# Optimization experiments

Hardware: AMD Instinct MI355X
Metric: run time of the kernel (lower is better)

Reference implementation:

```python
import jax, jax.numpy as jnp
import numpy as np

N, E = 50000, 800000
F_NODE, F_EDGE, H, LAT, MAXN = 128, 16, 128, 64, 200


def setup_inputs() -> dict:
    key = jax.random.key(0)
    ks = jax.random.split(key, 40)
    s = 0.05
    p = {
        'x': jax.random.normal(ks[0], (N, F_NODE), jnp.float32),
        'edge_index': jax.random.randint(ks[1], (2, E), 0, N, jnp.int64),
        'edge_attr': jax.random.normal(ks[2], (E, F_EDGE), jnp.float32),
        'eps': jax.random.normal(ks[3], (1, LAT), jnp.float32),
        'num_nodes': N,
        # GATConv layer 1 (heads=1)
        'W1': jax.random.normal(ks[4], (F_NODE, H), jnp.float32) * s,
        'att_src1': jax.random.normal(ks[5], (H,), jnp.float32) * s,
        'att_dst1': jax.random.normal(ks[6], (H,), jnp.float32) * s,
        'We1': jax.random.normal(ks[7], (F_EDGE, H), jnp.float32) * s,
        'att_e1': jax.random.normal(ks[8], (H,), jnp.float32) * s,
        'b1': jnp.zeros((H,), jnp.float32),
        # GATConv layer 2
        'W2': jax.random.normal(ks[9], (H, H), jnp.float32) * s,
        'att_src2': jax.random.normal(ks[10], (H,), jnp.float32) * s,
        'att_dst2': jax.random.normal(ks[11], (H,), jnp.float32) * s,
        'We2': jax.random.normal(ks[12], (F_EDGE, H), jnp.float32) * s,
        'att_e2': jax.random.normal(ks[13], (H,), jnp.float32) * s,
        'b2': jnp.zeros((H,), jnp.float32),
        # heads
        'mu_W': jax.random.normal(ks[14], (H, LAT), jnp.float32) * s,
        'mu_b': jnp.zeros((LAT,), jnp.float32),
        'lv_W': jax.random.normal(ks[15], (H, LAT), jnp.float32) * s,
        'lv_b': jnp.zeros((LAT,), jnp.float32),
        'dec_W': jax.random.normal(ks[16], (LAT, H), jnp.float32) * s,
        'dec_b': jnp.zeros((H,), jnp.float32),
        'adj_W1': jax.random.normal(ks[17], (H, H), jnp.float32) * s,
        'adj_b1': jnp.zeros((H,), jnp.float32),
        'adj_W2': jax.random.normal(ks[18], (H, MAXN), jnp.float32) * s,
        'adj_b2': jnp.zeros((MAXN,), jnp.float32),
        'nd_W1': jax.random.normal(ks[19], (H, H), jnp.float32) * s,
        'nd_b1': jnp.zeros((H,), jnp.float32),
        'nd_W2': jax.random.normal(ks[20], (H, F_NODE), jnp.float32) * s,
        'nd_b2': jnp.zeros((F_NODE,), jnp.float32),
    }
    return p


def _gat(h, src, dst, ea, W, a_s, a_d, We, a_e, b, n):
    # PyG GATConv, heads=1: linear transform, per-edge attention, segment softmax over dst
    g = h @ W                                     # [n, H]
    alpha = jax.nn.leaky_relu((g @ a_s)[src] + (g @ a_d)[dst] + (ea @ We) @ a_e,
                              negative_slope=0.2)  # [E']
    m = jax.ops.segment_max(alpha, dst, num_segments=n)
    ex = jnp.exp(alpha - m[dst])
    den = jax.ops.segment_sum(ex, dst, num_segments=n)
    w = ex / den[dst]
    return jax.ops.segment_sum(w[:, None] * g[src], dst, num_segments=n) + b


def _forward(x, edge_index, edge_attr, eps, num_nodes,
             W1, att_src1, att_dst1, We1, att_e1, b1,
             W2, att_src2, att_dst2, We2, att_e2, b2,
             mu_W, mu_b, lv_W, lv_b, dec_W, dec_b,
             adj_W1, adj_b1, adj_W2, adj_b2, nd_W1, nd_b1, nd_W2, nd_b2):
    n = x.shape[0]
    src, dst = edge_index[0], edge_index[1]
    # add self loops; self-loop edge_attr = per-node mean of incoming edge_attr (PyG fill_value='mean')
    deg = jax.ops.segment_sum(jnp.ones((src.shape[0],), x.dtype), dst, num_segments=n)
    mean_ea = jax.ops.segment_sum(edge_attr, dst, num_segments=n) / jnp.maximum(deg, 1.0)[:, None]
    loop = jnp.arange(n)
    src_f = jnp.concatenate([src, loop])
    dst_f = jnp.concatenate([dst, loop])
    ea_f = jnp.concatenate([edge_attr, mean_ea])
    h = jax.nn.relu(_gat(x, src_f, dst_f, ea_f, W1, att_src1, att_dst1, We1, att_e1, b1, n))
    h = jax.nn.relu(_gat(h, src_f, dst_f, ea_f, W2, att_src2, att_dst2, We2, att_e2, b2, n))
    hg = h.mean(axis=0, keepdims=True)            # global_mean_pool, single graph -> [1, H]
    mu = hg @ mu_W + mu_b
    logvar = hg @ lv_W + lv_b
    z = mu + eps * jnp.exp(0.5 * logvar)
    hd = jax.nn.relu(z @ dec_W + dec_b)           # [1, H]
    hn = jnp.broadcast_to(hd[:, None, :], (1, num_nodes, hd.shape[-1]))
    adj = jax.nn.relu(hn @ adj_W1 + adj_b1) @ adj_W2 + adj_b2   # [1, n, MAXN]
    adj = adj[:, :, :num_nodes]
    nodes = jax.nn.relu(hn @ nd_W1 + nd_b1) @ nd_W2 + nd_b2     # [1, n, F_NODE]
    return adj, nodes, mu, logvar


def reference(x, edge_index, edge_attr, eps, num_nodes,
              W1, att_src1, att_dst1, We1, att_e1, b1,
              W2, att_src2, att_dst2, We2, att_e2, b2,
              mu_W, mu_b, lv_W, lv_b, dec_W, dec_b,
              adj_W1, adj_b1, adj_W2, adj_b2, nd_W1, nd_b1, nd_W2, nd_b2):
    return _forward(x, edge_index, edge_attr, eps, num_nodes,
                    W1, att_src1, att_dst1, We1, att_e1, b1,
                    W2, att_src2, att_dst2, We2, att_e2, b2,
                    mu_W, mu_b, lv_W, lv_b, dec_W, dec_b,
                    adj_W1, adj_b1, adj_W2, adj_b2, nd_W1, nd_b1, nd_W2, nd_b2)
```

## Files before the change

kernel.cpp:

```cpp
#include <hip/hip_runtime.h>
#include <math.h>

#define NN   50000
#define EE   800000
#define EF   850000
#define HH   128
#define FE   16
#define LATD 64
#define MAXNN 200

#define ADJ_TOT   10000000
#define NODES_TOT 6400000
#define OUT_TOT   16400000
#define MU_OFF    16400000
#define LV_OFF    16400064

#define GEMMBLOCKS 782
#define DEGBLOCKS  782
#define NBSCAN     49
#define FLAGBIT    0x80000000u

typedef __attribute__((ext_vector_type(8))) short bf16x8;
typedef __attribute__((ext_vector_type(4))) float f32x4;
typedef __attribute__((ext_vector_type(2))) float f32x2;

__device__ __forceinline__ unsigned short f2bf(float f){
  unsigned int u = __float_as_uint(f);
  unsigned int r = (u + 0x7FFFu + ((u>>16)&1u)) >> 16;
  return (unsigned short)r;
}
__device__ __forceinline__ float bf2f(unsigned short h){
  return __uint_as_float(((unsigned int)h)<<16);
}

__global__ __launch_bounds__(256) void kprep(int* ideg, float* hgsum, unsigned* scanpub,
                       const float* We1, const float* ae1, const float* We2, const float* ae2,
                       float* wa1, float* wa2,
                       const float* W1, const float* W2,
                       unsigned short* Wp1, unsigned short* Wp2){
  int i = blockIdx.x*256 + threadIdx.x;
  if(i < NN) ideg[i]=0;
  if(i < HH) hgsum[i]=0.f;
  if(i < 64) scanpub[i]=0u;
  if(i < FE){
    float s1=0.f, s2=0.f;
    for(int j=0;j<HH;j++){ s1 += We1[i*HH+j]*ae1[j]; s2 += We2[i*HH+j]*ae2[j]; }
    wa1[i]=s1; wa2[i]=s2;
  }
  if(i < HH*HH){
    int n = i >> 7, k = i & 127;
    Wp1[i] = f2bf(W1[k*HH + n]);
    Wp2[i] = f2bf(W2[k*HH + n]);
  }
}

__device__ __forceinline__ void gemm_body(int bid, int tid, const void* __restrict__ hin, int h_is_fp32,
    const unsigned short* __restrict__ Wp,
    const float* __restrict__ atts, const float* __restrict__ attd,
    unsigned char* __restrict__ A8, float* __restrict__ asrc, float* __restrict__ adst){
  int lane = tid & 63;
  int wid  = tid >> 6;
  int l = lane & 15, q = lane >> 4;
  int r0 = bid*64 + wid*16;
  if(r0 >= NN) return;
  const unsigned short* hb = (const unsigned short*)hin;
  const float*          hf = (const float*)hin;
  int row = r0 + l;

  bf16x8 afr[4];
  if(h_is_fp32){
    float4 u[8];
    #pragma unroll
    for(int kb=0;kb<4;kb++){
      const float* p = hf + (size_t)row*HH + kb*32 + q*8;
      u[kb*2]   = *(const float4*)(p);
      u[kb*2+1] = *(const float4*)(p+4);
    }
    #pragma unroll
    for(int kb=0;kb<4;kb++){
      afr[kb][0]=(short)f2bf(u[kb*2].x);   afr[kb][1]=(short)f2bf(u[kb*2].y);
      afr[kb][2]=(short)f2bf(u[kb*2].z);   afr[kb][3]=(short)f2bf(u[kb*2].w);
      afr[kb][4]=(short)f2bf(u[kb*2+1].x); afr[kb][5]=(short)f2bf(u[kb*2+1].y);
      afr[kb][6]=(short)f2bf(u[kb*2+1].z); afr[kb][7]=(short)f2bf(u[kb*2+1].w);
    }
  } else {
    #pragma unroll
    for(int kb=0;kb<4;kb++)
      afr[kb] = *(const bf16x8*)(hb + (size_t)row*HH + kb*32 + q*8);
  }

  f32x4 acc[8];
  #pragma unroll
  for(int t=0;t<8;t++) acc[t]=(f32x4){0.f,0.f,0.f,0.f};

  #pragma unroll
  for(int kb=0;kb<4;kb++){
    #pragma unroll
    for(int t=0;t<8;t++){
      bf16x8 b = *(const bf16x8*)(Wp + (size_t)(t*16+l)*HH + kb*32 + q*8);
      acc[t] = __builtin_amdgcn_mfma_f32_16x16x32_bf16(afr[kb], b, acc[t], 0,0,0);
    }
  }

  float av[8], dv[8];
  #pragma unroll
  for(int t=0;t<8;t++){ av[t]=atts[t*16+l]; dv[t]=attd[t*16+l]; }
  #pragma unroll
  for(int reg=0;reg<4;reg++){
    float ps=0.f, pd=0.f;
    #pragma unroll
    for(int t=0;t<8;t++){ ps+=acc[t][reg]*av[t]; pd+=acc[t][reg]*dv[t]; }
    #pragma unroll
    for(int m=8;m>=1;m>>=1){ ps+=__shfl_xor(ps,m,16); pd+=__shfl_xor(pd,m,16); }
    if(l==0){ int R=r0+q*4+reg; asrc[R]=ps; adst[R]=pd; }
  }
  #pragma unroll
  for(int t=0;t<8;t++)
    #pragma unroll
    for(int reg=0;reg<4;reg++){
      int pk = __builtin_amdgcn_cvt_pk_fp8_f32(acc[t][reg], 0.f, 0, false);
      A8[(size_t)(r0+q*4+reg)*HH + t*16 + l] = (unsigned char)(pk & 0xFF);
    }
}

__global__ __launch_bounds__(256) void kgemm3(const void* __restrict__ hin, int h_is_fp32,
    const unsigned short* __restrict__ Wp,
    const float* __restrict__ atts, const float* __restrict__ attd,
    unsigned char* __restrict__ A8, float* __restrict__ asrc, float* __restrict__ adst){
  gemm_body(blockIdx.x, threadIdx.x, hin, h_is_fp32, Wp, atts, attd, A8, asrc, adst);
}

__device__ __forceinline__ unsigned etpack(const float4* a4,
                         const float* __restrict__ wa1, const float* __restrict__ wa2){
  float4 v0=a4[0], v1=a4[1], v2=a4[2], v3=a4[3];
  float va[16]={v0.x,v0.y,v0.z,v0.w, v1.x,v1.y,v1.z,v1.w,
                v2.x,v2.y,v2.z,v2.w, v3.x,v3.y,v3.z,v3.w};
  float d1=0.f,d2=0.f;
  #pragma unroll
  for(int f=0;f<FE;f++){ d1+=va[f]*wa1[f]; d2+=va[f]*wa2[f]; }
  return (unsigned)f2bf(d1) | ((unsigned)f2bf(d2)<<16);
}

__global__ __launch_bounds__(256) void kdeggemm(
    const int* __restrict__ ei, int* ideg, unsigned short* __restrict__ erank,
    const float* __restrict__ ea, const float* __restrict__ wa1, const float* __restrict__ wa2,
    unsigned* __restrict__ ety,
    const void* __restrict__ hin, int h_is_fp32,
    const unsigned short* __restrict__ Wp,
    const float* __restrict__ atts, const float* __restrict__ attd,
    unsigned char* __restrict__ A8, float* __restrict__ asrc, float* __restrict__ adst){
  if(blockIdx.x < GEMMBLOCKS){
    gemm_body(blockIdx.x, threadIdx.x, hin, h_is_fp32, Wp, atts, attd, A8, asrc, adst);
  } else {
    int e0 = ((blockIdx.x - GEMMBLOCKS)*256 + threadIdx.x)*4;
    if(e0 + 3 < EE){
      int4 d4 = *(const int4*)(ei + EE + e0);
      unsigned short r0 = (unsigned short)atomicAdd(&ideg[d4.x], 1);
      unsigned short r1 = (unsigned short)atomicAdd(&ideg[d4.y], 1);
      unsigned short r2 = (unsigned short)atomicAdd(&ideg[d4.z], 1);
      unsigned short r3 = (unsigned short)atomicAdd(&ideg[d4.w], 1);
      const float4* a4 = (const float4*)(ea + (size_t)e0*FE);
      uint4 y;
      y.x = etpack(a4,    wa1, wa2);
      y.y = etpack(a4+4,  wa1, wa2);
      y.z = etpack(a4+8,  wa1, wa2);
      y.w = etpack(a4+12, wa1, wa2);
      *(uint4*)(ety + e0) = y;
      ushort4 rr; rr.x=r0; rr.y=r1; rr.z=r2; rr.w=r3;
      *(ushort4*)(erank + e0) = rr;
    }
  }
}

__global__ void kscanf(const int* __restrict__ ideg, int* __restrict__ rowstart,
                       unsigned* __restrict__ scanpub){
  __shared__ int sd[1024];
  __shared__ int bo[64];
  int t=threadIdx.x, b=blockIdx.x;
  int i = b*1024 + t;
  int v = (i<NN)? (ideg[i]+1) : 0;
  sd[t]=v; __syncthreads();
  for(int off=1; off<1024; off<<=1){
    int x=(t>=off)? sd[t-off]:0; __syncthreads();
    sd[t]+=x; __syncthreads();
  }
  if(t==1023) atomicExch(&scanpub[b], (unsigned)sd[1023] | FLAGBIT);
  if(t<64){
    int j = (t<NBSCAN)? t : NBSCAN-1;
    unsigned u;
    do { u = atomicAdd(&scanpub[j], 0u); } while(!(u & FLAGBIT));
    int agg = (t<NBSCAN)? (int)(u & ~FLAGBIT) : 0;
    int inc = agg;
    #pragma unroll
    for(int off=1; off<64; off<<=1){
      int x = __shfl_up(inc, off);
      if(t>=off) inc += x;
    }
    bo[t] = inc - agg;
  }
  __syncthreads();
  if(i<NN) rowstart[i] = sd[t]-v + bo[b];
  if(b==0 && t==0) rowstart[NN] = bo[NBSCAN];
}

__global__ __launch_bounds__(256) void kscatter(const int* __restrict__ ei,
                         const unsigned* __restrict__ ety,
                         const int* __restrict__ rowstart,
                         const unsigned short* __restrict__ erank,
                         uint2* __restrict__ csr){
  int e0 = (blockIdx.x*256 + threadIdx.x)*4;
  if(e0 >= EE) return;
  int4 s4 = *(const int4*)(ei + e0);
  int4 d4 = *(const int4*)(ei + EE + e0);
  ushort4 r4 = *(const ushort4*)(erank + e0);
  uint4 y4 = *(const uint4*)(ety + e0);
  uint2 en;
  en.x=(unsigned)s4.x; en.y=y4.x; csr[rowstart[d4.x]+(int)r4.x]=en;
  en.x=(unsigned)s4.y; en.y=y4.y; csr[rowstart[d4.y]+(int)r4.y]=en;
  en.x=(unsigned)s4.z; en.y=y4.z; csr[rowstart[d4.z]+(int)r4.z]=en;
  en.x=(unsigned)s4.w; en.y=y4.w; csr[rowstart[d4.w]+(int)r4.w]=en;
}

__global__ __launch_bounds__(256) void kgat(const unsigned char* __restrict__ A8,
    const float* __restrict__ asrc, const float* __restrict__ adst,
    const int* __restrict__ rowstart, uint2* __restrict__ csr,
    int mode, const float* __restrict__ bias,
    float* __restrict__ alphabuf, int* __restrict__ srcbuf,
    unsigned short* __restrict__ Bout){
  int lane = threadIdx.x & 63;
  int wid  = threadIdx.x >> 6;
  int half = lane >> 5;
  int hl   = lane & 31;
  int i = blockIdx.x*8 + wid*2 + half;
  if(i >= NN) return;
  int base = rowstart[i];
  int len  = rowstart[i+1]-base;
  float adi = adst[i];
  int lq = hl & 15;
  int qq = hl >> 4;
  float av[8];
  #pragma unroll
  for(int j=0;j<8;j++) av[j]=0.f;

  if(__builtin_expect(len <= 32, 1)){
    int P2 = (len+1)>>1;
    int nread = mode ? len : len-1;
    int s = i; float etlo = 0.f, ethi = 0.f;
    if(hl < nread){
      uint2 en = csr[base+hl];
      s = (int)en.x;
      etlo = bf2f((unsigned short)(en.y & 0xFFFFu));
      ethi = bf2f((unsigned short)(en.y >> 16));
    }
    float et = mode ? ethi : etlo;
    int skv0[6];
    #pragma unroll
    for(int j=0;j<6;j++) skv0[j] = (j<P2) ? __shfl(s, 2*j+qq, 32) : i;
    unsigned ux[6], uy[6];
    #pragma unroll
    for(int j=0;j<6;j++){
      uint2 u = *(const uint2*)(A8 + (size_t)skv0[j]*HH + lq*8);
      ux[j]=u.x; uy[j]=u.y;
    }
    if(!mode){
      float e1 = (hl < len-1) ? etlo : 0.f;
      float e2 = (hl < len-1) ? ethi : 0.f;
      #pragma unroll
      for(int mk=16;mk>=1;mk>>=1){ e1 += __shfl_xor(e1,mk); e2 += __shfl_xor(e2,mk); }
      float dg = fmaxf((float)(len-1), 1.f);
      float m1 = e1/dg, m2 = e2/dg;
      if(hl == len-1){
        et = m1;
        uint2 se; se.x=(unsigned)i;
        se.y=(unsigned)f2bf(m1) | ((unsigned)f2bf(m2)<<16);
        csr[base+len-1] = se;
      }
    }
    float a = -1e30f;
    if(hl < len){
      a = asrc[s] + adi + et;
      a = fmaxf(a, 0.2f*a);
    }
    float m = a;
    #pragma unroll
    for(int mk=16;mk>=1;mk>>=1) m = fmaxf(m, __shfl_xor(m,mk));
    float ex = (hl<len) ? __expf(a-m) : 0.f;
    float sm = ex;
    #pragma unroll
    for(int mk=16;mk>=1;mk>>=1) sm += __shfl_xor(sm,mk);
    ex *= __builtin_amdgcn_rcpf(sm);

    float w0[6];
    #pragma unroll
    for(int j=0;j<6;j++) w0[j] = (j<P2) ? __shfl(ex, 2*j+qq, 32) : 0.f;
    #pragma unroll
    for(int j=0;j<6;j++){
      f32x2 v;
      v=__builtin_amdgcn_cvt_pk_f32_fp8((int)ux[j],false); av[0]+=w0[j]*v[0]; av[1]+=w0[j]*v[1];
      v=__builtin_amdgcn_cvt_pk_f32_fp8((int)ux[j],true ); av[2]+=w0[j]*v[0]; av[3]+=w0[j]*v[1];
      v=__builtin_amdgcn_cvt_pk_f32_fp8((int)uy[j],false); av[4]+=w0[j]*v[0]; av[5]+=w0[j]*v[1];
      v=__builtin_amdgcn_cvt_pk_f32_fp8((int)uy[j],true ); av[6]+=w0[j]*v[0]; av[7]+=w0[j]*v[1];
    }
    for(int t0=6; t0<P2; t0+=6){
      int skv[6]; float w[6];
      #pragma unroll
      for(int j=0;j<6;j++){
        if(t0+j < P2){
          int idx = 2*(t0+j) + qq;
          skv[j] = __shfl(s, idx, 32);
          w[j]   = __shfl(ex, idx, 32);
        } else { skv[j] = i; w[j] = 0.f; }
      }
      unsigned vx[6], vy[6];
      #pragma unroll
      for(int j=0;j<6;j++){
        uint2 u = *(const uint2*)(A8 + (size_t)skv[j]*HH + lq*8);
        vx[j]=u.x; vy[j]=u.y;
      }
      #pragma unroll
      for(int j=0;j<6;j++){
        f32x2 v;
        v=__builtin_amdgcn_cvt_pk_f32_fp8((int)vx[j],false); av[0]+=w[j]*v[0]; av[1]+=w[j]*v[1];
        v=__builtin_amdgcn_cvt_pk_f32_fp8((int)vx[j],true ); av[2]+=w[j]*v[0]; av[3]+=w[j]*v[1];
        v=__builtin_amdgcn_cvt_pk_f32_fp8((int)vy[j],false); av[4]+=w[j]*v[0]; av[5]+=w[j]*v[1];
        v=__builtin_amdgcn_cvt_pk_f32_fp8((int)vy[j],true ); av[6]+=w[j]*v[0]; av[7]+=w[j]*v[1];
      }
    }
  } else {
    int deg = len-1;
    int lim = mode ? len : deg;
    float lm = -1e30f, e1 = 0.f, e2 = 0.f;
    for(int k=hl;k<lim;k+=32){
      uint2 en = csr[base+k];
      int sr = (int)en.x;
      float lo = bf2f((unsigned short)(en.y & 0xFFFFu));
      float hi = bf2f((unsigned short)(en.y >> 16));
      float etv = mode ? hi : lo;
      if(!mode){ e1 += lo; e2 += hi; }
      float a = asrc[sr] + adi + etv;
      a = fmaxf(a, 0.2f*a);
      alphabuf[base+k]=a; srcbuf[base+k]=sr;
      lm = fmaxf(lm,a);
    }
    #pragma unroll
    for(int mk=16;mk>=1;mk>>=1){
      e1 += __shfl_xor(e1,mk);
      e2 += __shfl_xor(e2,mk);
      lm  = fmaxf(lm, __shfl_xor(lm,mk));
    }
    float aself = 0.f;
    if(!mode){
      float m1 = e1/(float)deg, m2 = e2/(float)deg;
      aself = asrc[i] + adi + m1;
      aself = fmaxf(aself, 0.2f*aself);
      lm = fmaxf(lm, aself);
      if(hl==0){
        uint2 se; se.x=(unsigned)i;
        se.y=(unsigned)f2bf(m1) | ((unsigned)f2bf(m2)<<16);
        csr[base+deg] = se;
      }
    }
    float ls=0.f;
    for(int k=hl;k<len;k+=32){
      float a;
      if(mode) a = alphabuf[base+k];
      else     a = (k<deg)? alphabuf[base+k] : aself;
      float e_ = __expf(a-lm);
      alphabuf[base+k]=e_;
      ls += e_;
    }
    #pragma unroll
    for(int mk=16;mk>=1;mk>>=1) ls += __shfl_xor(ls,mk);
    float inv = 1.f/ls;
    int lim2 = mode ? len : deg;
    int P2 = (len+1)>>1;
    for(int t=0;t<P2;t++){
      int k = 2*t + qq;
      int sk = i; float wk = 0.f;
      if(k<len){
        sk = (k<lim2)? srcbuf[base+k] : i;
        wk = alphabuf[base+k]*inv;
      }
      uint2 u = *(const uint2*)(A8 + (size_t)sk*HH + lq*8);
      f32x2 v;
      v=__builtin_amdgcn_cvt_pk_f32_fp8((int)u.x,false); av[0]+=wk*v[0]; av[1]+=wk*v[1];
      v=__builtin_amdgcn_cvt_pk_f32_fp8((int)u.x,true ); av[2]+=wk*v[0]; av[3]+=wk*v[1];
      v=__builtin_amdgcn_cvt_pk_f32_fp8((int)u.y,false); av[4]+=wk*v[0]; av[5]+=wk*v[1];
      v=__builtin_amdgcn_cvt_pk_f32_fp8((int)u.y,true ); av[6]+=wk*v[0]; av[7]+=wk*v[1];
    }
  }

  #pragma unroll
  for(int j=0;j<8;j++) av[j] += __shfl_xor(av[j],16);
  if(qq==0){
    const float4* bp = (const float4*)(bias + lq*8);
    float4 b0=bp[0], b1=bp[1];
    float o0=fmaxf(av[0]+b0.x,0.f), o1=fmaxf(av[1]+b0.y,0.f);
    float o2=fmaxf(av[2]+b0.z,0.f), o3=fmaxf(av[3]+b0.w,0.f);
    float o4=fmaxf(av[4]+b1.x,0.f), o5=fmaxf(av[5]+b1.y,0.f);
    float o6=fmaxf(av[6]+b1.z,0.f), o7=fmaxf(av[7]+b1.w,0.f);
    uint4 ov;
    ov.x=(unsigned)f2bf(o0)|((unsigned)f2bf(o1)<<16);
    ov.y=(unsigned)f2bf(o2)|((unsigned)f2bf(o3)<<16);
    ov.z=(unsigned)f2bf(o4)|((unsigned)f2bf(o5)<<16);
    ov.w=(unsigned)f2bf(o6)|((unsigned)f2bf(o7)<<16);
    *(uint4*)(Bout + (size_t)i*HH + lq*8) = ov;
  }
}

__global__ __launch_bounds__(256) void khg(const unsigned short* __restrict__ B, float* hgsum){
  int f = threadIdx.x & 127;
  int half = threadIdx.x >> 7;
  float s=0.f;
  for(int i = blockIdx.x*2+half; i < NN; i += gridDim.x*2)
    s += bf2f(B[(size_t)i*HH + f]);
  __shared__ float sd[256];
  sd[threadIdx.x]=s; __syncthreads();
  if(half==0) atomicAdd(&hgsum[f], sd[threadIdx.x]+sd[threadIdx.x+128]);
}

__global__ __launch_bounds__(256) void kdec(const float* __restrict__ hgsum, const float* __restrict__ eps,
   const float* muW,const float* mub,const float* lvW,const float* lvb,
   const float* decW,const float* decb,
   const float* aW1,const float* ab1,const float* aW2,const float* ab2,
   const float* nW1,const float* nb1,const float* nW2,const float* nb2,
   float* out, float* rowadj, float* rownodes){
  __shared__ float hg[HH], z[LATD], hd[HH], t1[HH], t2[HH];
  int t=threadIdx.x;
  if(t<HH) hg[t]=hgsum[t]*(1.0f/NN);
  __syncthreads();
  if(t<LATD){
    float mu=mub[t], lv=lvb[t];
    #pragma unroll 8
    for(int k=0;k<HH;k++){ mu += hg[k]*muW[k*LATD+t]; lv += hg[k]*lvW[k*LATD+t]; }
    out[MU_OFF+t]=mu; out[LV_OFF+t]=lv;
    z[t]=mu + eps[t]*expf(0.5f*lv);
  }
  __syncthreads();
  if(t<HH){
    float a=decb[t];
    #pragma unroll 8
    for(int k=0;k<LATD;k++) a += z[k]*decW[k*HH+t];
    hd[t]=fmaxf(a,0.f);
  }
  __syncthreads();
  if(t<HH){
    float a=ab1[t];
    #pragma unroll 8
    for(int k=0;k<HH;k++) a += hd[k]*aW1[k*HH+t];
    t1[t]=fmaxf(a,0.f);
  } else {
    int j=t-HH;
    float a=nb1[j];
    #pragma unroll 8
    for(int k=0;k<HH;k++) a += hd[k]*nW1[k*HH+j];
    t2[j]=fmaxf(a,0.f);
  }
  __syncthreads();
  for(int j=t;j<MAXNN;j+=256){
    float a=ab2[j];
    #pragma unroll 8
    for(int k=0;k<HH;k++) a += t1[k]*aW2[k*MAXNN+j];
    rowadj[j]=a;
  }
  if(t<HH){
    float a=nb2[t];
    #pragma unroll 8
    for(int k=0;k<HH;k++) a += t2[k]*nW2[k*HH+t];
    rownodes[t]=a;
  }
}

__global__ __launch_bounds__(256) void kbcast(const float* __restrict__ rowadj,
                                              const float* __restrict__ rownodes,
                                              float* __restrict__ out){
  int lane = threadIdx.x & 63;
  int wv = (blockIdx.x*256 + threadIdx.x) >> 6;
  int nw = (gridDim.x*256) >> 6;
  float4 aseg = {0.f,0.f,0.f,0.f}, nseg = {0.f,0.f,0.f,0.f};
  if(lane<50) aseg = ((const float4*)rowadj)[lane];
  if(lane<32) nseg = ((const float4*)rownodes)[lane];
  for(int r=wv; r<NN; r+=nw)
    if(lane<50) *(float4*)(out + (size_t)r*MAXNN + lane*4) = aseg;
  for(int r=wv; r<NN; r+=nw)
    if(lane<32) *(float4*)(out + ADJ_TOT + (size_t)r*HH + lane*4) = nseg;
}

extern "C" void kernel_launch(void* const* d_in, const int* in_sizes, int n_in,
                              void* d_out, int out_size, void* d_ws, size_t ws_size,
                              hipStream_t stream){
  const float* x   = (const float*)d_in[0];
  const int*   ei  = (const int*)d_in[1];
  const float* ea  = (const float*)d_in[2];
  const float* eps = (const float*)d_in[3];
  const float* W1  =(const float*)d_in[5];
  const float* as1 =(const float*)d_in[6];
  const float* ad1 =(const float*)d_in[7];
  const float* We1 =(const float*)d_in[8];
  const float* ae1 =(const float*)d_in[9];
  const float* b1  =(const float*)d_in[10];
  const float* W2  =(const float*)d_in[11];
  const float* as2 =(const float*)d_in[12];
  const float* ad2 =(const float*)d_in[13];
  const float* We2 =(const float*)d_in[14];
  const float* ae2 =(const float*)d_in[15];
  const float* b2  =(const float*)d_in[16];
  const float* muW =(const float*)d_in[17];
  const float* mub =(const float*)d_in[18];
  const float* lvW =(const float*)d_in[19];
  const float* lvb =(const float*)d_in[20];
  const float* decW=(const float*)d_in[21];
  const float* decb=(const float*)d_in[22];
  const float* aW1 =(const float*)d_in[23];
  const float* ab1 =(const float*)d_in[24];
  const float* aW2 =(const float*)d_in[25];
  const float* ab2 =(const float*)d_in[26];
  const float* nW1 =(const float*)d_in[27];
  const float* nb1 =(const float*)d_in[28];
  const float* nW2 =(const float*)d_in[29];
  const float* nb2 =(const float*)d_in[30];
  float* out=(float*)d_out;

  char* w=(char*)d_ws;
  unsigned char*  A8  = (unsigned char*)w;  w += (size_t)NN*HH;
  unsigned short* Bbf = (unsigned short*)w; w += (size_t)NN*HH*2;
  unsigned short* Wp1 = (unsigned short*)w; w += (size_t)HH*HH*2;
  unsigned short* Wp2 = (unsigned short*)w; w += (size_t)HH*HH*2;
  uint2*  csr      = (uint2*)w;  w += (size_t)EF*8;
  float*  alphabuf = (float*)w;  w += (size_t)EF*4;
  int*    srcbuf   = (int*)w;    w += (size_t)EF*4;
  unsigned* ety    = (unsigned*)w; w += (size_t)EE*4;
  unsigned short* erank = (unsigned short*)w; w += (size_t)EE*2;
  int*    rowstart = (int*)w;    w += (size_t)(NN+1)*4;
  int*    ideg     = (int*)w;    w += (size_t)NN*4;
  float*  hgsum    = (float*)w;  w += 128*4;
  float*  asrc     = (float*)w;  w += (size_t)NN*4;
  float*  adst     = (float*)w;  w += (size_t)NN*4;
  float*  wa1      = (float*)w;  w += 16*4;
  float*  wa2      = (float*)w;  w += 16*4;
  float*  rowadj   = (float*)w;  w += 256*4;
  float*  rownodes = (float*)w;  w += 128*4;
  unsigned* scanpub= (unsigned*)w; w += 64*4;

  int gatblocks  = (NN+7)/8;

  hipLaunchKernelGGL(kprep, dim3((NN+255)/256), dim3(256), 0, stream,
                     ideg, hgsum, scanpub, We1, ae1, We2, ae2, wa1, wa2, W1, W2, Wp1, Wp2);
  hipLaunchKernelGGL(kdeggemm, dim3(GEMMBLOCKS+DEGBLOCKS), dim3(256), 0, stream,
                     ei, ideg, erank, ea, wa1, wa2, ety,
                     (const void*)x, 1, Wp1, as1, ad1, A8, asrc, adst);
  hipLaunchKernelGGL(kscanf, dim3(NBSCAN), dim3(1024), 0, stream, ideg, rowstart, scanpub);
  hipLaunchKernelGGL(kscatter, dim3((EE/4+255)/256), dim3(256), 0, stream,
                     ei, ety, rowstart, erank, csr);
  hipLaunchKernelGGL(kgat,  dim3(gatblocks), dim3(256), 0, stream,
                     A8, asrc, adst, rowstart, csr, 0, b1, alphabuf, srcbuf, Bbf);
  hipLaunchKernelGGL(kgemm3, dim3(GEMMBLOCKS), dim3(256), 0, stream,
                     (const void*)Bbf, 0, Wp2, as2, ad2, A8, asrc, adst);
  hipLaunchKernelGGL(kgat,  dim3(gatblocks), dim3(256), 0, stream,
                     A8, asrc, adst, rowstart, csr, 1, b2, alphabuf, srcbuf, Bbf);
  hipLaunchKernelGGL(khg,   dim3(512), dim3(256), 0, stream, Bbf, hgsum);
  hipLaunchKernelGGL(kdec,  dim3(1), dim3(256), 0, stream, hgsum, eps,
                     muW,mub,lvW,lvb,decW,decb,aW1,ab1,aW2,ab2,nW1,nb1,nW2,nb2,
                     out, rowadj, rownodes);
  hipLaunchKernelGGL(kbcast, dim3(2048), dim3(256), 0, stream, rowadj, rownodes, out);
}
```

Measured before the change: 399.0 us.

## Fuse whole pipeline into one cooperative persistent kernel with grid syncs

Replaces the chain of ten kernel launches with a single cooperative kernel that loops blocks over work units and separates stages with grid-wide syncs. The lookback scan becomes a two-level chunk scan, and the edge-attribute projection moves from the degree pass into the scatter pass, which drops the ety buffer. The intent is to cut launch gaps and tail effects between stages. In exchange, grid syncs add barrier cost, the persistent grid is capped by occupancy, and register pressure from the merged body may lower occupancy for the GAT and GEMM stages. A multi-kernel fallback is kept for devices without cooperative launch.

Result: slower. 862.0 us (+116.0%).

```diff
diff --git a/kernel.cpp b/kernel.cpp
--- a/kernel.cpp
+++ b/kernel.cpp
@@ -1,22 +1,26 @@
 #include <hip/hip_runtime.h>
+#include <hip/hip_cooperative_groups.h>
 #include <math.h>
+
+namespace cg = cooperative_groups;
 
 #define NN   50000
 #define EE   800000
-#define EF   850000
 #define HH   128
 #define FE   16
 #define LATD 64
 #define MAXNN 200
 
 #define ADJ_TOT   10000000
-#define NODES_TOT 6400000
 #define OUT_TOT   16400000
 #define MU_OFF    16400000
 #define LV_OFF    16400064
 
 #define GEMMBLOCKS 782
 #define DEGBLOCKS  782
+#define SCATUNITS  1563
+#define GATUNITS   6250
+#define NCHUNK     196
 #define NBSCAN     49
 #define FLAGBIT    0x80000000u
 
@@ -33,26 +37,6 @@
   return __uint_as_float(((unsigned int)h)<<16);
 }
 
-__global__ __launch_bounds__(256) void kprep(int* ideg, float* hgsum, unsigned* scanpub,
-                       const float* We1, const float* ae1, const float* We2, const float* ae2,
-                       float* wa1, float* wa2,
-                       const float* W1, const float* W2,
-                       unsigned short* Wp1, unsigned short* Wp2){
-  int i = blockIdx.x*256 + threadIdx.x;
-  if(i < NN) ideg[i]=0;
-  if(i < HH) hgsum[i]=0.f;
-  if(i < 64) scanpub[i]=0u;
-  if(i < FE){
-    float s1=0.f, s2=0.f;
-    for(int j=0;j<HH;j++){ s1 += We1[i*HH+j]*ae1[j]; s2 += We2[i*HH+j]*ae2[j]; }
-    wa1[i]=s1; wa2[i]=s2;
-  }
-  if(i < HH*HH){
-    int n = i >> 7, k = i & 127;
-    Wp1[i] = f2bf(W1[k*HH + n]);
-    Wp2[i] = f2bf(W2[k*HH + n]);
-  }
-}
 
 __device__ __forceinline__ void gemm_body(int bid, int tid, const void* __restrict__ hin, int h_is_fp32,
     const unsigned short* __restrict__ Wp,
@@ -123,11 +107,18 @@
     }
 }
 
-__global__ __launch_bounds__(256) void kgemm3(const void* __restrict__ hin, int h_is_fp32,
-    const unsigned short* __restrict__ Wp,
-    const float* __restrict__ atts, const float* __restrict__ attd,
-    unsigned char* __restrict__ A8, float* __restrict__ asrc, float* __restrict__ adst){
-  gemm_body(blockIdx.x, threadIdx.x, hin, h_is_fp32, Wp, atts, attd, A8, asrc, adst);
+__device__ __forceinline__ void deg_unit(int u, int tid,
+    const int* __restrict__ ei, int* ideg, unsigned short* __restrict__ erank){
+  int e0 = (u*256 + tid)*4;
+  if(e0 + 3 < EE){
+    int4 d4 = *(const int4*)(ei + EE + e0);
+    unsigned short r0 = (unsigned short)atomicAdd(&ideg[d4.x], 1);
+    unsigned short r1 = (unsigned short)atomicAdd(&ideg[d4.y], 1);
+    unsigned short r2 = (unsigned short)atomicAdd(&ideg[d4.z], 1);
+    unsigned short r3 = (unsigned short)atomicAdd(&ideg[d4.w], 1);
+    ushort4 rr; rr.x=r0; rr.y=r1; rr.z=r2; rr.w=r3;
+    *(ushort4*)(erank + e0) = rr;
+  }
 }
 
 __device__ __forceinline__ unsigned etpack(const float4* a4,
@@ -141,97 +132,36 @@
   return (unsigned)f2bf(d1) | ((unsigned)f2bf(d2)<<16);
 }
 
-__global__ __launch_bounds__(256) void kdeggemm(
-    const int* __restrict__ ei, int* ideg, unsigned short* __restrict__ erank,
-    const float* __restrict__ ea, const float* __restrict__ wa1, const float* __restrict__ wa2,
-    unsigned* __restrict__ ety,
-    const void* __restrict__ hin, int h_is_fp32,
-    const unsigned short* __restrict__ Wp,
-    const float* __restrict__ atts, const float* __restrict__ attd,
-    unsigned char* __restrict__ A8, float* __restrict__ asrc, float* __restrict__ adst){
-  if(blockIdx.x < GEMMBLOCKS){
-    gemm_body(blockIdx.x, threadIdx.x, hin, h_is_fp32, Wp, atts, attd, A8, asrc, adst);
-  } else {
-    int e0 = ((blockIdx.x - GEMMBLOCKS)*256 + threadIdx.x)*4;
-    if(e0 + 3 < EE){
-      int4 d4 = *(const int4*)(ei + EE + e0);
-      unsigned short r0 = (unsigned short)atomicAdd(&ideg[d4.x], 1);
-      unsigned short r1 = (unsigned short)atomicAdd(&ideg[d4.y], 1);
-      unsigned short r2 = (unsigned short)atomicAdd(&ideg[d4.z], 1);
-      unsigned short r3 = (unsigned short)atomicAdd(&ideg[d4.w], 1);
-      const float4* a4 = (const float4*)(ea + (size_t)e0*FE);
-      uint4 y;
-      y.x = etpack(a4,    wa1, wa2);
-      y.y = etpack(a4+4,  wa1, wa2);
-      y.z = etpack(a4+8,  wa1, wa2);
-      y.w = etpack(a4+12, wa1, wa2);
-      *(uint4*)(ety + e0) = y;
-      ushort4 rr; rr.x=r0; rr.y=r1; rr.z=r2; rr.w=r3;
-      *(ushort4*)(erank + e0) = rr;
-    }
-  }
-}
-
-__global__ void kscanf(const int* __restrict__ ideg, int* __restrict__ rowstart,
-                       unsigned* __restrict__ scanpub){
-  __shared__ int sd[1024];
-  __shared__ int bo[64];
-  int t=threadIdx.x, b=blockIdx.x;
-  int i = b*1024 + t;
-  int v = (i<NN)? (ideg[i]+1) : 0;
-  sd[t]=v; __syncthreads();
-  for(int off=1; off<1024; off<<=1){
-    int x=(t>=off)? sd[t-off]:0; __syncthreads();
-    sd[t]+=x; __syncthreads();
-  }
-  if(t==1023) atomicExch(&scanpub[b], (unsigned)sd[1023] | FLAGBIT);
-  if(t<64){
-    int j = (t<NBSCAN)? t : NBSCAN-1;
-    unsigned u;
-    do { u = atomicAdd(&scanpub[j], 0u); } while(!(u & FLAGBIT));
-    int agg = (t<NBSCAN)? (int)(u & ~FLAGBIT) : 0;
-    int inc = agg;
-    #pragma unroll
-    for(int off=1; off<64; off<<=1){
-      int x = __shfl_up(inc, off);
-      if(t>=off) inc += x;
-    }
-    bo[t] = inc - agg;
-  }
-  __syncthreads();
-  if(i<NN) rowstart[i] = sd[t]-v + bo[b];
-  if(b==0 && t==0) rowstart[NN] = bo[NBSCAN];
-}
-
-__global__ __launch_bounds__(256) void kscatter(const int* __restrict__ ei,
-                         const unsigned* __restrict__ ety,
-                         const int* __restrict__ rowstart,
-                         const unsigned short* __restrict__ erank,
-                         uint2* __restrict__ csr){
-  int e0 = (blockIdx.x*256 + threadIdx.x)*4;
+__device__ __forceinline__ void scat_unit(int u, int tid,
+    const int* __restrict__ ei, const float* __restrict__ ea,
+    const float* __restrict__ wa1, const float* __restrict__ wa2,
+    const int* __restrict__ rowstart, const unsigned short* __restrict__ erank,
+    uint2* __restrict__ csr){
+  int e0 = (u*256 + tid)*2;
   if(e0 >= EE) return;
-  int4 s4 = *(const int4*)(ei + e0);
-  int4 d4 = *(const int4*)(ei + EE + e0);
-  ushort4 r4 = *(const ushort4*)(erank + e0);
-  uint4 y4 = *(const uint4*)(ety + e0);
-  uint2 en;
-  en.x=(unsigned)s4.x; en.y=y4.x; csr[rowstart[d4.x]+(int)r4.x]=en;
-  en.x=(unsigned)s4.y; en.y=y4.y; csr[rowstart[d4.y]+(int)r4.y]=en;
-  en.x=(unsigned)s4.z; en.y=y4.z; csr[rowstart[d4.z]+(int)r4.z]=en;
-  en.x=(unsigned)s4.w; en.y=y4.w; csr[rowstart[d4.w]+(int)r4.w]=en;
-}
-
-__global__ __launch_bounds__(256) void kgat(const unsigned char* __restrict__ A8,
+  int sA=ei[e0],    sB=ei[e0+1];
+  int dA=ei[EE+e0], dB=ei[EE+e0+1];
+  int rA=(int)erank[e0], rB=(int)erank[e0+1];
+  int pA=rowstart[dA]+rA, pB=rowstart[dB]+rB;
+  const float4* a4 = (const float4*)(ea + (size_t)e0*FE);
+  unsigned yA = etpack(a4,   wa1, wa2);
+  unsigned yB = etpack(a4+4, wa1, wa2);
+  uint2 enA; enA.x=(unsigned)sA; enA.y=yA;
+  uint2 enB; enB.x=(unsigned)sB; enB.y=yB;
+  csr[pA]=enA; csr[pB]=enB;
+}
+
+__device__ void kgat_body(int unit, int tid, const unsigned char* __restrict__ A8,
     const float* __restrict__ asrc, const float* __restrict__ adst,
     const int* __restrict__ rowstart, uint2* __restrict__ csr,
     int mode, const float* __restrict__ bias,
     float* __restrict__ alphabuf, int* __restrict__ srcbuf,
     unsigned short* __restrict__ Bout){
-  int lane = threadIdx.x & 63;
-  int wid  = threadIdx.x >> 6;
+  int lane = tid & 63;
+  int wid  = tid >> 6;
   int half = lane >> 5;
   int hl   = lane & 31;
-  int i = blockIdx.x*8 + wid*2 + half;
+  int i = unit*8 + wid*2 + half;
   if(i >= NN) return;
   int base = rowstart[i];
   int len  = rowstart[i+1]-base;
@@ -408,25 +338,26 @@
   }
 }
 
-__global__ __launch_bounds__(256) void khg(const unsigned short* __restrict__ B, float* hgsum){
-  int f = threadIdx.x & 127;
-  int half = threadIdx.x >> 7;
+__device__ __forceinline__ void khg_unit(int u, int tid,
+    const unsigned short* __restrict__ B, float* hgsum, float* sfd){
+  int f = tid & 127;
+  int half = tid >> 7;
   float s=0.f;
-  for(int i = blockIdx.x*2+half; i < NN; i += gridDim.x*2)
+  for(int i = u*2+half; i < NN; i += 1024)
     s += bf2f(B[(size_t)i*HH + f]);
-  __shared__ float sd[256];
-  sd[threadIdx.x]=s; __syncthreads();
-  if(half==0) atomicAdd(&hgsum[f], sd[threadIdx.x]+sd[threadIdx.x+128]);
-}
-
-__global__ __launch_bounds__(256) void kdec(const float* __restrict__ hgsum, const float* __restrict__ eps,
+  sfd[tid]=s; __syncthreads();
+  if(half==0) atomicAdd(&hgsum[f], sfd[tid]+sfd[tid+128]);
+  __syncthreads();
+}
+
+__device__ void dec_body(int tid, const float* __restrict__ hgsum, const float* __restrict__ eps,
    const float* muW,const float* mub,const float* lvW,const float* lvb,
    const float* decW,const float* decb,
    const float* aW1,const float* ab1,const float* aW2,const float* ab2,
    const float* nW1,const float* nb1,const float* nW2,const float* nb2,
-   float* out, float* rowadj, float* rownodes){
-  __shared__ float hg[HH], z[LATD], hd[HH], t1[HH], t2[HH];
-  int t=threadIdx.x;
+   float* out, float* rowadj, float* rownodes,
+   float* hg, float* z, float* hd, float* t1, float* t2){
+  int t=tid;
   if(t<HH) hg[t]=hgsum[t]*(1.0f/NN);
   __syncthreads();
   if(t<LATD){
@@ -471,12 +402,9 @@
   }
 }
 
-__global__ __launch_bounds__(256) void kbcast(const float* __restrict__ rowadj,
-                                              const float* __restrict__ rownodes,
-                                              float* __restrict__ out){
-  int lane = threadIdx.x & 63;
-  int wv = (blockIdx.x*256 + threadIdx.x) >> 6;
-  int nw = (gridDim.x*256) >> 6;
+__device__ __forceinline__ void bcast_wave(int wv, int nw, int lane,
+    const float* __restrict__ rowadj, const float* __restrict__ rownodes,
+    float* __restrict__ out){
   float4 aseg = {0.f,0.f,0.f,0.f}, nseg = {0.f,0.f,0.f,0.f};
   if(lane<50) aseg = ((const float4*)rowadj)[lane];
   if(lane<32) nseg = ((const float4*)rownodes)[lane];
@@ -485,6 +413,210 @@
   for(int r=wv; r<NN; r+=nw)
     if(lane<32) *(float4*)(out + ADJ_TOT + (size_t)r*HH + lane*4) = nseg;
 }
+
+
+struct MP {
+  const float *x; const int *ei; const float *ea; const float *eps;
+  const float *W1,*as1,*ad1,*We1,*ae1,*b1;
+  const float *W2,*as2,*ad2,*We2,*ae2,*b2;
+  const float *muW,*mub,*lvW,*lvb,*decW,*decb;
+  const float *aW1,*ab1,*aW2,*ab2,*nW1,*nb1,*nW2,*nb2;
+  float *out;
+  unsigned char *A8; unsigned short *Bbf, *Wp1, *Wp2;
+  uint2 *csr; float *alphabuf; int *srcbuf; unsigned short *erank;
+  int *rowstart, *ideg; float *hgsum, *asrc, *adst, *wa1, *wa2, *rowadj, *rownodes;
+  int *chunksum, *chunkoff;
+};
+
+__global__ __launch_bounds__(256) void kmega(MP p){
+  cg::grid_group grid = cg::this_grid();
+  const int nb  = gridDim.x;
+  const int tid = threadIdx.x;
+  const int gid = blockIdx.x*256 + tid;
+  const int gsz = nb*256;
+  __shared__ int   sd[256];
+  __shared__ float sfd[256];
+  __shared__ float shg[HH], sz[LATD], shd[HH], st1[HH], st2[HH];
+
+  for(int i=gid; i<NN; i+=gsz) p.ideg[i]=0;
+  for(int i=gid; i<HH; i+=gsz) p.hgsum[i]=0.f;
+  for(int i=gid; i<FE; i+=gsz){
+    float s1=0.f, s2=0.f;
+    for(int j=0;j<HH;j++){ s1 += p.We1[i*HH+j]*p.ae1[j]; s2 += p.We2[i*HH+j]*p.ae2[j]; }
+    p.wa1[i]=s1; p.wa2[i]=s2;
+  }
+  for(int i=gid; i<HH*HH; i+=gsz){
+    int n = i >> 7, k = i & 127;
+    p.Wp1[i] = f2bf(p.W1[k*HH + n]);
+    p.Wp2[i] = f2bf(p.W2[k*HH + n]);
+  }
+  grid.sync();
+  for(int bu=blockIdx.x; bu<GEMMBLOCKS+DEGBLOCKS; bu+=nb){
+    if(bu < GEMMBLOCKS) gemm_body(bu, tid, (const void*)p.x, 1, p.Wp1, p.as1, p.ad1, p.A8, p.asrc, p.adst);
+    else                deg_unit(bu-GEMMBLOCKS, tid, p.ei, p.ideg, p.erank);
+  }
+  grid.sync();
+  for(int u=blockIdx.x; u<NCHUNK; u+=nb){
+    __syncthreads();
+    int i = u*256 + tid;
+    int v = (i<NN)? (p.ideg[i]+1) : 0;
+    sd[tid]=v; __syncthreads();
+    for(int off=1; off<256; off<<=1){
+      int xv=(tid>=off)? sd[tid-off]:0; __syncthreads();
+      sd[tid]+=xv; __syncthreads();
+    }
+    if(i<NN) p.rowstart[i] = sd[tid]-v;
+    if(tid==255) p.chunksum[u]=sd[255];
+  }
+  grid.sync();
+  if(blockIdx.x==0){
+    int v = (tid<NCHUNK)? p.chunksum[tid] : 0;
+    sd[tid]=v; __syncthreads();
+    for(int off=1; off<256; off<<=1){
+      int xv=(tid>=off)? sd[tid-off]:0; __syncthreads();
+      sd[tid]+=xv; __syncthreads();
+    }
+    p.chunkoff[tid] = sd[tid]-v;
+    if(tid==255) p.rowstart[NN] = sd[255];
+  }
+  grid.sync();
+  for(int i=gid; i<NN; i+=gsz) p.rowstart[i] += p.chunkoff[i>>8];
+  grid.sync();
+  for(int u=blockIdx.x; u<SCATUNITS; u+=nb)
+    scat_unit(u, tid, p.ei, p.ea, p.wa1, p.wa2, p.rowstart, p.erank, p.csr);
+  grid.sync();
+  for(int u=blockIdx.x; u<GATUNITS; u+=nb)
+    kgat_body(u, tid, p.A8, p.asrc, p.adst, p.rowstart, p.csr, 0, p.b1, p.alphabuf, p.srcbuf, p.Bbf);
+  grid.sync();
+  for(int bu=blockIdx.x; bu<GEMMBLOCKS; bu+=nb)
+    gemm_body(bu, tid, (const void*)p.Bbf, 0, p.Wp2, p.as2, p.ad2, p.A8, p.asrc, p.adst);
+  grid.sync();
+  for(int u=blockIdx.x; u<GATUNITS; u+=nb)
+    kgat_body(u, tid, p.A8, p.asrc, p.adst, p.rowstart, p.csr, 1, p.b2, p.alphabuf, p.srcbuf, p.Bbf);
+  grid.sync();
+  for(int u=blockIdx.x; u<512; u+=nb)
+    khg_unit(u, tid, p.Bbf, p.hgsum, sfd);
+  grid.sync();
+  if(blockIdx.x==0)
+    dec_body(tid, p.hgsum, p.eps, p.muW,p.mub,p.lvW,p.lvb,p.decW,p.decb,
+             p.aW1,p.ab1,p.aW2,p.ab2,p.nW1,p.nb1,p.nW2,p.nb2,
+             p.out, p.rowadj, p.rownodes, shg, sz, shd, st1, st2);
+  grid.sync();
+  bcast_wave(gid>>6, gsz>>6, tid&63, p.rowadj, p.rownodes, p.out);
+}
+
+
+__global__ __launch_bounds__(256) void kprep(int* ideg, float* hgsum, unsigned* scanpub,
+                       const float* We1, const float* ae1, const float* We2, const float* ae2,
+                       float* wa1, float* wa2,
+                       const float* W1, const float* W2,
+                       unsigned short* Wp1, unsigned short* Wp2){
+  int i = blockIdx.x*256 + threadIdx.x;
+  if(i < NN) ideg[i]=0;
+  if(i < HH) hgsum[i]=0.f;
+  if(i < 64) scanpub[i]=0u;
+  if(i < FE){
+    float s1=0.f, s2=0.f;
+    for(int j=0;j<HH;j++){ s1 += We1[i*HH+j]*ae1[j]; s2 += We2[i*HH+j]*ae2[j]; }
+    wa1[i]=s1; wa2[i]=s2;
+  }
+  if(i < HH*HH){
+    int n = i >> 7, k = i & 127;
+    Wp1[i] = f2bf(W1[k*HH + n]);
+    Wp2[i] = f2bf(W2[k*HH + n]);
+  }
+}
+
+__global__ __launch_bounds__(256) void kdeggemm(
+    const int* __restrict__ ei, int* ideg, unsigned short* __restrict__ erank,
+    const void* __restrict__ hin, int h_is_fp32,
+    const unsigned short* __restrict__ Wp,
+    const float* __restrict__ atts, const float* __restrict__ attd,
+    unsigned char* __restrict__ A8, float* __restrict__ asrc, float* __restrict__ adst){
+  if(blockIdx.x < GEMMBLOCKS)
+    gemm_body(blockIdx.x, threadIdx.x, hin, h_is_fp32, Wp, atts, attd, A8, asrc, adst);
+  else
+    deg_unit(blockIdx.x-GEMMBLOCKS, threadIdx.x, ei, ideg, erank);
+}
+
+__global__ void kscanf(const int* __restrict__ ideg, int* __restrict__ rowstart,
+                       unsigned* __restrict__ scanpub){
+  __shared__ int sd[1024];
+  __shared__ int bo[64];
+  int t=threadIdx.x, b=blockIdx.x;
+  int i = b*1024 + t;
+  int v = (i<NN)? (ideg[i]+1) : 0;
+  sd[t]=v; __syncthreads();
+  for(int off=1; off<1024; off<<=1){
+    int x=(t>=off)? sd[t-off]:0; __syncthreads();
+    sd[t]+=x; __syncthreads();
+  }
+  if(t==1023) atomicExch(&scanpub[b], (unsigned)sd[1023] | FLAGBIT);
+  if(t<64){
+    int j = (t<NBSCAN)? t : NBSCAN-1;
+    unsigned u;
+    do { u = atomicAdd(&scanpub[j], 0u); } while(!(u & FLAGBIT));
+    int agg = (t<NBSCAN)? (int)(u & ~FLAGBIT) : 0;
+    int inc = agg;
+    #pragma unroll
+    for(int off=1; off<64; off<<=1){
+      int x = __shfl_up(inc, off);
+      if(t>=off) inc += x;
+    }
+    bo[t] = inc - agg;
+  }
+  __syncthreads();
+  if(i<NN) rowstart[i] = sd[t]-v + bo[b];
+  if(b==0 && t==0) rowstart[NN] = bo[NBSCAN];
+}
+
+__global__ __launch_bounds__(256) void kscatter(const int* __restrict__ ei, const float* __restrict__ ea,
+                         const float* __restrict__ wa1, const float* __restrict__ wa2,
+                         const int* __restrict__ rowstart, const unsigned short* __restrict__ erank,
+                         uint2* __restrict__ csr){
+  scat_unit(blockIdx.x, threadIdx.x, ei, ea, wa1, wa2, rowstart, erank, csr);
+}
+
+__global__ __launch_bounds__(256) void kgat(const unsigned char* __restrict__ A8,
+    const float* __restrict__ asrc, const float* __restrict__ adst,
+    const int* __restrict__ rowstart, uint2* __restrict__ csr,
+    int mode, const float* __restrict__ bias,
+    float* __restrict__ alphabuf, int* __restrict__ srcbuf,
+    unsigned short* __restrict__ Bout){
+  kgat_body(blockIdx.x, threadIdx.x, A8, asrc, adst, rowstart, csr, mode, bias, alphabuf, srcbuf, Bout);
+}
+
+__global__ __launch_bounds__(256) void kgemm3(const void* __restrict__ hin, int h_is_fp32,
+    const unsigned short* __restrict__ Wp,
+    const float* __restrict__ atts, const float* __restrict__ attd,
+    unsigned char* __restrict__ A8, float* __restrict__ asrc, float* __restrict__ adst){
+  gemm_body(blockIdx.x, threadIdx.x, hin, h_is_fp32, Wp, atts, attd, A8, asrc, adst);
+}
+
+__global__ __launch_bounds__(256) void khg(const unsigned short* __restrict__ B, float* hgsum){
+  __shared__ float sfd[256];
+  khg_unit(blockIdx.x, threadIdx.x, B, hgsum, sfd);
+}
+
+__global__ __launch_bounds__(256) void kdec(const float* __restrict__ hgsum, const float* __restrict__ eps,
+   const float* muW,const float* mub,const float* lvW,const float* lvb,
+   const float* decW,const float* decb,
+   const float* aW1,const float* ab1,const float* aW2,const float* ab2,
+   const float* nW1,const float* nb1,const float* nW2,const float* nb2,
+   float* out, float* rowadj, float* rownodes){
+  __shared__ float hg[HH], z[LATD], hd[HH], t1[HH], t2[HH];
+  dec_body(threadIdx.x, hgsum, eps, muW,mub,lvW,lvb,decW,decb,
+           aW1,ab1,aW2,ab2,nW1,nb1,nW2,nb2, out, rowadj, rownodes, hg,z,hd,t1,t2);
+}
+
+__global__ __launch_bounds__(256) void kbcast(const float* __restrict__ rowadj,
+                                              const float* __restrict__ rownodes,
+                                              float* __restrict__ out){
+  int wv = (blockIdx.x*256 + threadIdx.x) >> 6;
+  int nw = (gridDim.x*256) >> 6;
+  bcast_wave(wv, nw, threadIdx.x & 63, rowadj, rownodes, out);
+}
+
 
 extern "C" void kernel_launch(void* const* d_in, const int* in_sizes, int n_in,
                               void* d_out, int out_size, void* d_ws, size_t ws_size,
@@ -526,10 +658,9 @@
   unsigned short* Bbf = (unsigned short*)w; w += (size_t)NN*HH*2;
   unsigned short* Wp1 = (unsigned short*)w; w += (size_t)HH*HH*2;
   unsigned short* Wp2 = (unsigned short*)w; w += (size_t)HH*HH*2;
-  uint2*  csr      = (uint2*)w;  w += (size_t)EF*8;
-  float*  alphabuf = (float*)w;  w += (size_t)EF*4;
-  int*    srcbuf   = (int*)w;    w += (size_t)EF*4;
-  unsigned* ety    = (unsigned*)w; w += (size_t)EE*4;
+  uint2*  csr      = (uint2*)w;  w += (size_t)(EE+NN)*8;
+  float*  alphabuf = (float*)w;  w += (size_t)(EE+NN)*4;
+  int*    srcbuf   = (int*)w;    w += (size_t)(EE+NN)*4;
   unsigned short* erank = (unsigned short*)w; w += (size_t)EE*2;
   int*    rowstart = (int*)w;    w += (size_t)(NN+1)*4;
   int*    ideg     = (int*)w;    w += (size_t)NN*4;
@@ -541,26 +672,54 @@
   float*  rowadj   = (float*)w;  w += 256*4;
   float*  rownodes = (float*)w;  w += 128*4;
   unsigned* scanpub= (unsigned*)w; w += 64*4;
-
-  int gatblocks  = (NN+7)/8;
-
-  hipLaunchKernelGGL(kprep, dim3((NN+255)/256), dim3(256), 0, stream,
-                     ideg, hgsum, scanpub, We1, ae1, We2, ae2, wa1, wa2, W1, W2, Wp1, Wp2);
-  hipLaunchKernelGGL(kdeggemm, dim3(GEMMBLOCKS+DEGBLOCKS), dim3(256), 0, stream,
-                     ei, ideg, erank, ea, wa1, wa2, ety,
-                     (const void*)x, 1, Wp1, as1, ad1, A8, asrc, adst);
-  hipLaunchKernelGGL(kscanf, dim3(NBSCAN), dim3(1024), 0, stream, ideg, rowstart, scanpub);
-  hipLaunchKernelGGL(kscatter, dim3((EE/4+255)/256), dim3(256), 0, stream,
-                     ei, ety, rowstart, erank, csr);
-  hipLaunchKernelGGL(kgat,  dim3(gatblocks), dim3(256), 0, stream,
-                     A8, asrc, adst, rowstart, csr, 0, b1, alphabuf, srcbuf, Bbf);
-  hipLaunchKernelGGL(kgemm3, dim3(GEMMBLOCKS), dim3(256), 0, stream,
-                     (const void*)Bbf, 0, Wp2, as2, ad2, A8, asrc, adst);
-  hipLaunchKernelGGL(kgat,  dim3(gatblocks), dim3(256), 0, stream,
-                     A8, asrc, adst, rowstart, csr, 1, b2, alphabuf, srcbuf, Bbf);
-  hipLaunchKernelGGL(khg,   dim3(512), dim3(256), 0, stream, Bbf, hgsum);
-  hipLaunchKernelGGL(kdec,  dim3(1), dim3(256), 0, stream, hgsum, eps,
-                     muW,mub,lvW,lvb,decW,decb,aW1,ab1,aW2,ab2,nW1,nb1,nW2,nb2,
-                     out, rowadj, rownodes);
-  hipLaunchKernelGGL(kbcast, dim3(2048), dim3(256), 0, stream, rowadj, rownodes, out);
-}
+  int*    chunksum = (int*)w;    w += 256*4;
+  int*    chunkoff = (int*)w;    w += 257*4;
+
+  static int coopGrid = -1;
+  if(coopGrid < 0){
+    int cl=0, ncu=0, mab=0;
+    hipDeviceGetAttribute(&cl, hipDeviceAttributeCooperativeLaunch, 0);
+    hipDeviceGetAttribute(&ncu, hipDeviceAttributeMultiprocessorCount, 0);
+    hipOccupancyMaxActiveBlocksPerMultiprocessor(&mab, kmega, 256, 0);
+    int g = (cl && mab>0) ? mab*ncu : 0;
+    if(g > 2048) g = 2048;
+    coopGrid = (g >= 128) ? g : 0;
+  }
+
+  if(coopGrid > 0){
+    MP p;
+    p.x=x; p.ei=ei; p.ea=ea; p.eps=eps;
+    p.W1=W1; p.as1=as1; p.ad1=ad1; p.We1=We1; p.ae1=ae1; p.b1=b1;
+    p.W2=W2; p.as2=as2; p.ad2=ad2; p.We2=We2; p.ae2=ae2; p.b2=b2;
+    p.muW=muW; p.mub=mub; p.lvW=lvW; p.lvb=lvb; p.decW=decW; p.decb=decb;
+    p.aW1=aW1; p.ab1=ab1; p.aW2=aW2; p.ab2=ab2; p.nW1=nW1; p.nb1=nb1; p.nW2=nW2; p.nb2=nb2;
+    p.out=out;
+    p.A8=A8; p.Bbf=Bbf; p.Wp1=Wp1; p.Wp2=Wp2;
+    p.csr=csr; p.alphabuf=alphabuf; p.srcbuf=srcbuf; p.erank=erank;
+    p.rowstart=rowstart; p.ideg=ideg; p.hgsum=hgsum; p.asrc=asrc; p.adst=adst;
+    p.wa1=wa1; p.wa2=wa2; p.rowadj=rowadj; p.rownodes=rownodes;
+    p.chunksum=chunksum; p.chunkoff=chunkoff;
+    void* args[] = { (void*)&p };
+    hipLaunchCooperativeKernel((const void*)kmega, dim3(coopGrid), dim3(256), args, 0, stream);
+  } else {
+    int gatblocks = GATUNITS;
+    hipLaunchKernelGGL(kprep, dim3((NN+255)/256), dim3(256), 0, stream,
+                       ideg, hgsum, scanpub, We1, ae1, We2, ae2, wa1, wa2, W1, W2, Wp1, Wp2);
+    hipLaunchKernelGGL(kdeggemm, dim3(GEMMBLOCKS+DEGBLOCKS), dim3(256), 0, stream,
+                       ei, ideg, erank, (const void*)x, 1, Wp1, as1, ad1, A8, asrc, adst);
+    hipLaunchKernelGGL(kscanf, dim3(NBSCAN), dim3(1024), 0, stream, ideg, rowstart, scanpub);
+    hipLaunchKernelGGL(kscatter, dim3(SCATUNITS), dim3(256), 0, stream,
+                       ei, ea, wa1, wa2, rowstart, erank, csr);
+    hipLaunchKernelGGL(kgat,  dim3(gatblocks), dim3(256), 0, stream,
+                       A8, asrc, adst, rowstart, csr, 0, b1, alphabuf, srcbuf, Bbf);
+    hipLaunchKernelGGL(kgemm3, dim3(GEMMBLOCKS), dim3(256), 0, stream,
+                       (const void*)Bbf, 0, Wp2, as2, ad2, A8, asrc, adst);
+    hipLaunchKernelGGL(kgat,  dim3(gatblocks), dim3(256), 0, stream,
+                       A8, asrc, adst, rowstart, csr, 1, b2, alphabuf, srcbuf, Bbf);
+    hipLaunchKernelGGL(khg,   dim3(512), dim3(256), 0, stream, Bbf, hgsum);
+    hipLaunchKernelGGL(kdec,  dim3(1), dim3(256), 0, stream, hgsum, eps,
+                       muW,mub,lvW,lvb,decW,decb,aW1,ab1,aW2,ab2,nW1,nb1,nW2,nb2,
+                       out, rowadj, rownodes);
+    hipLaunchKernelGGL(kbcast, dim3(2048), dim3(256), 0, stream, rowadj, rownodes, out);
+  }
+}
```
